# Kernel optimization log

Measured on AMD Instinct MI355X. Metric: run time of the kernel, lower is better.

The kernel has to match this reference:

```python
import jax, jax.numpy as jnp
import numpy as np

D, HEADS, HD, L, P, DFF = 256, 8, 32, 4, 4, 2048
B, NQ = 4, 900
SHAPES = [(128, 128), (64, 64), (32, 32), (16, 16)]
S = sum(h * w for h, w in SHAPES)


def setup_inputs():
    ks = iter(jax.random.split(jax.random.key(0), 20))
    rn = lambda *s: jax.random.normal(next(ks), s, jnp.float32) * 0.02
    cxcy = jax.random.uniform(next(ks), (B, NQ, 1, 2), minval=0.1, maxval=0.9)
    wh = jax.random.uniform(next(ks), (B, NQ, 1, 2), minval=0.05, maxval=0.3)
    ref = jnp.broadcast_to(jnp.concatenate([cxcy, wh], -1), (B, NQ, L, 4))
    starts = np.cumsum([0] + [h * w for h, w in SHAPES[:-1]])
    return dict(
        query=jax.random.normal(next(ks), (B, NQ, D), jnp.float32),
        query_pos=jax.random.normal(next(ks), (B, NQ, D), jnp.float32),
        reference_points=ref,
        input_flatten=jax.random.normal(next(ks), (B, S, D), jnp.float32),
        input_spatial_shapes=jnp.array(SHAPES, jnp.int32),
        input_level_start_index=jnp.array(starts, jnp.int32),
        sa_in_w=rn(3, D, D), sa_in_b=jnp.zeros((3, D)),
        sa_out_w=rn(D, D), sa_out_b=jnp.zeros((D,)),
        norm1_g=jnp.ones((D,)), norm1_b=jnp.zeros((D,)),
        value_w=rn(D, D), value_b=jnp.zeros((D,)),
        off_w=rn(D, HEADS * L * P * 2),
        off_b=jax.random.uniform(next(ks), (HEADS * L * P * 2,), minval=-1.0, maxval=1.0),
        aw_w=rn(D, HEADS * L * P), aw_b=jnp.zeros((HEADS * L * P,)),
        ca_out_w=rn(D, D), ca_out_b=jnp.zeros((D,)),
        norm2_g=jnp.ones((D,)), norm2_b=jnp.zeros((D,)),
        lin1_w=rn(D, DFF), lin1_b=jnp.zeros((DFF,)),
        lin2_w=rn(DFF, D), lin2_b=jnp.zeros((D,)),
        norm3_g=jnp.ones((D,)), norm3_b=jnp.zeros((D,)),
    )


def _ln(x, g, b, eps=1e-5):
    m = x.mean(-1, keepdims=True)
    v = ((x - m) ** 2).mean(-1, keepdims=True)
    return (x - m) * jax.lax.rsqrt(v + eps) * g + b


def _msdeform(q, input_flatten, ref, shapes, starts, value_w, value_b,
              off_w, off_b, aw_w, aw_b, out_w, out_b):
    Bq, Nq, _ = q.shape
    # value: (B, heads, S, head_dim)
    v = (input_flatten @ value_w + value_b).reshape(Bq, -1, HEADS, HD).transpose(0, 2, 1, 3)
    off = (q @ off_w + off_b).reshape(Bq, Nq, HEADS, L, P, 2).transpose(0, 2, 1, 3, 4, 5)
    aw = jax.nn.softmax((q @ aw_w + aw_b).reshape(Bq, Nq, HEADS, L * P), axis=-1)
    aw = aw.reshape(Bq, Nq, HEADS, L, P).transpose(0, 2, 1, 3, 4)  # (B,H,Nq,L,P)
    refc = ref[:, None, :, :, None, :]  # (B,1,Nq,L,1,4)
    # box refs: center + offset/P * wh * 0.5  (Deformable-DETR convention)
    loc = refc[..., :2] + off / P * refc[..., 2:] * 0.5  # (B,H,Nq,L,P,2)
    out = jnp.zeros((Bq, HEADS, Nq, HD), q.dtype)
    for l, (H, W) in enumerate(shapes):
        vl = jax.lax.dynamic_slice_in_dim(v, starts[l], H * W, axis=2)  # (B,H,HW,hd)
        x = loc[:, :, :, l, :, 0] * W - 0.5  # align_corners=False pixel coords
        y = loc[:, :, :, l, :, 1] * H - 0.5
        x0, y0 = jnp.floor(x), jnp.floor(y)
        dx, dy = x - x0, y - y0

        def g(xi, yi):
            valid = (xi >= 0) & (xi < W) & (yi >= 0) & (yi < H)  # zero padding
            idx = (jnp.clip(yi, 0, H - 1) * W + jnp.clip(xi, 0, W - 1)).astype(jnp.int32)
            gat = jnp.take_along_axis(vl, idx.reshape(Bq, HEADS, Nq * P, 1), axis=2)
            return gat.reshape(Bq, HEADS, Nq, P, HD) * valid[..., None]

        samp = (((1 - dx) * (1 - dy))[..., None] * g(x0, y0)
                + (dx * (1 - dy))[..., None] * g(x0 + 1, y0)
                + ((1 - dx) * dy)[..., None] * g(x0, y0 + 1)
                + (dx * dy)[..., None] * g(x0 + 1, y0 + 1))
        out = out + jnp.sum(aw[:, :, :, l, :, None] * samp, axis=3)
    return out.transpose(0, 2, 1, 3).reshape(Bq, Nq, D) @ out_w + out_b


def _layer(query, query_pos, reference_points, input_flatten, shapes, starts, p):
    Bq, Nq, _ = query.shape
    qk = query + query_pos
    heads = lambda x: x.reshape(Bq, Nq, HEADS, HD).transpose(0, 2, 1, 3)
    qh = heads(qk @ p['sa_in_w'][0] + p['sa_in_b'][0])
    kh = heads(qk @ p['sa_in_w'][1] + p['sa_in_b'][1])
    vh = heads(query @ p['sa_in_w'][2] + p['sa_in_b'][2])
    attn = jax.nn.softmax(jnp.einsum('bhqd,bhkd->bhqk', qh, kh) * (HD ** -0.5), axis=-1)
    sa = jnp.einsum('bhqk,bhkd->bhqd', attn, vh).transpose(0, 2, 1, 3).reshape(Bq, Nq, D)
    sa = sa @ p['sa_out_w'] + p['sa_out_b']
    x = _ln(query + sa, p['norm1_g'], p['norm1_b'])
    ca = _msdeform(x + query_pos, input_flatten, reference_points, shapes, starts,
                   p['value_w'], p['value_b'], p['off_w'], p['off_b'],
                   p['aw_w'], p['aw_b'], p['ca_out_w'], p['ca_out_b'])
    x = _ln(x + ca, p['norm2_g'], p['norm2_b'])
    ffn = jax.nn.relu(x @ p['lin1_w'] + p['lin1_b']) @ p['lin2_w'] + p['lin2_b']
    return _ln(x + ffn, p['norm3_g'], p['norm3_b'])


PNAMES = ['sa_in_w', 'sa_in_b', 'sa_out_w', 'sa_out_b', 'norm1_g', 'norm1_b',
          'value_w', 'value_b', 'off_w', 'off_b', 'aw_w', 'aw_b',
          'ca_out_w', 'ca_out_b', 'norm2_g', 'norm2_b',
          'lin1_w', 'lin1_b', 'lin2_w', 'lin2_b', 'norm3_g', 'norm3_b']


def reference(query, query_pos, reference_points, input_flatten,
              input_spatial_shapes, input_level_start_index,
              sa_in_w, sa_in_b, sa_out_w, sa_out_b, norm1_g, norm1_b,
              value_w, value_b, off_w, off_b, aw_w, aw_b,
              ca_out_w, ca_out_b, norm2_g, norm2_b,
              lin1_w, lin1_b, lin2_w, lin2_b, norm3_g, norm3_b):
    # spatial shapes / start indices are static structural metadata
    shapes = [(int(h), int(w)) for h, w in np.asarray(input_spatial_shapes)]
    starts = [int(s) for s in np.asarray(input_level_start_index)]
    p = dict(zip(PNAMES, (sa_in_w, sa_in_b, sa_out_w, sa_out_b, norm1_g, norm1_b,
                          value_w, value_b, off_w, off_b, aw_w, aw_b,
                          ca_out_w, ca_out_b, norm2_g, norm2_b,
                          lin1_w, lin1_b, lin2_w, lin2_b, norm3_g, norm3_b)))
    return _layer(query, query_pos, reference_points, input_flatten, shapes, starts, p)
```

## Files before the change

kernel.cpp:

```cpp
#include <hip/hip_runtime.h>
#include <hip/hip_bf16.h>

#define DD   256
#define NH   8
#define HDIM 32
#define LV   4
#define NP   4
#define DFF  2048
#define BB   4
#define NQQ  900
#define SS   21760

typedef __bf16 bf16x8 __attribute__((ext_vector_type(8)));
typedef __bf16 bf16x2 __attribute__((ext_vector_type(2)));
typedef float  f32x4  __attribute__((ext_vector_type(4)));

__device__ inline void stval(float* p, float v) { *p = v; }
__device__ inline void stval(__bf16* p, float v) { *p = (__bf16)v; }

struct TPtrs {
    const float* s[10];
    __bf16* d[10];
};

__global__ void transp_all(TPtrs P) {
    const int Ks[10] = {256, 256, 256, 256, 256, 256, 256, 256, 256, 2048};
    const int Ns[10] = {256, 256, 256, 256, 256, 256, 128, 256, 2048, 256};
    const int tiles[10] = {64, 64, 64, 64, 64, 64, 32, 64, 512, 512};
    int t = blockIdx.x;
    int j = 0, base = 0;
    while (t >= base + tiles[j]) { base += tiles[j]; j++; }
    int lt = t - base;
    int K = Ks[j], N = Ns[j];
    int tn = N >> 5;
    int nb = (lt % tn) * 32, kb = (lt / tn) * 32;
    const float* W = P.s[j];
    __bf16* Wt = P.d[j];
    __shared__ float tbuf[32][33];
    for (int i = threadIdx.y; i < 32; i += 8)
        tbuf[i][threadIdx.x] = W[(size_t)(kb + i) * N + nb + threadIdx.x];
    __syncthreads();
    for (int i = threadIdx.y; i < 32; i += 8)
        Wt[(size_t)(nb + i) * K + kb + threadIdx.x] = (__bf16)tbuf[threadIdx.x][i];
}

#define BM 64
#define BN 64
#define BKK 64

template <typename AT, typename OT, int RELU, int NSUB>
__global__ __launch_bounds__(256) void mfma_gemm(
    const AT* __restrict__ A, const float* __restrict__ A2,
    const __bf16* __restrict__ Wt,
    const float* __restrict__ bias, const float* __restrict__ bias2, int nsplit,
    OT* __restrict__ C, int M, int N, int K) {
    int tid = threadIdx.x;
    int lane = tid & 63;
    int wave = tid >> 6;
    int wr = wave >> 1, wc = wave & 1;
    int m0 = blockIdx.y * BM;
    int n0 = blockIdx.x * (BN * NSUB);

    __shared__ __attribute__((aligned(16))) __bf16 As[BM * BKK];
    __shared__ __attribute__((aligned(16))) __bf16 Bs[NSUB][BN * BKK];

    f32x4 acc[NSUB][2][2] = {};

    int srow = tid >> 2;
    int sq = tid & 3;
    int u0 = sq << 1;
    int p0 = (u0 ^ (srow & 7)) * 8;
    int p1 = ((u0 + 1) ^ (srow & 7)) * 8;
    int fr = lane & 15, gq = lane >> 4;

    for (int k0 = 0; k0 < K; k0 += BKK) {
        {
            int gm = m0 + srow;
            bf16x8 v0 = {}, v1 = {};
            if (gm < M) {
                if constexpr (sizeof(AT) == 4) {
                    const float* ap = (const float*)A + (size_t)gm * K + k0 + sq * 16;
                    f32x4 f0 = *(const f32x4*)(ap + 0);
                    f32x4 f1 = *(const f32x4*)(ap + 4);
                    f32x4 f2 = *(const f32x4*)(ap + 8);
                    f32x4 f3 = *(const f32x4*)(ap + 12);
                    if (A2) {
                        const float* ap2 = A2 + (size_t)gm * K + k0 + sq * 16;
                        f0 += *(const f32x4*)(ap2 + 0);
                        f1 += *(const f32x4*)(ap2 + 4);
                        f2 += *(const f32x4*)(ap2 + 8);
                        f3 += *(const f32x4*)(ap2 + 12);
                    }
#pragma unroll
                    for (int e = 0; e < 4; e++) {
                        v0[e] = (__bf16)f0[e]; v0[e + 4] = (__bf16)f1[e];
                        v1[e] = (__bf16)f2[e]; v1[e + 4] = (__bf16)f3[e];
                    }
                } else {
                    const __bf16* ap = (const __bf16*)A + (size_t)gm * K + k0 + sq * 16;
                    v0 = *(const bf16x8*)(ap);
                    v1 = *(const bf16x8*)(ap + 8);
                }
            }
            *(bf16x8*)(&As[srow * 64 + p0]) = v0;
            *(bf16x8*)(&As[srow * 64 + p1]) = v1;
        }
#pragma unroll
        for (int ns = 0; ns < NSUB; ns++) {
            int gn = n0 + ns * BN + srow;
            const __bf16* bp = Wt + (size_t)gn * K + k0 + sq * 16;
            bf16x8 w0 = *(const bf16x8*)(bp);
            bf16x8 w1 = *(const bf16x8*)(bp + 8);
            *(bf16x8*)(&Bs[ns][srow * 64 + p0]) = w0;
            *(bf16x8*)(&Bs[ns][srow * 64 + p1]) = w1;
        }
        __syncthreads();
#pragma unroll
        for (int ks = 0; ks < 2; ks++) {
            bf16x8 a[2];
#pragma unroll
            for (int i = 0; i < 2; i++) {
                int ma = wr * 32 + i * 16 + fr;
                a[i] = *(const bf16x8*)(&As[ma * 64 + ((ks * 4 + gq) ^ (ma & 7)) * 8]);
            }
#pragma unroll
            for (int ns = 0; ns < NSUB; ns++) {
                bf16x8 b[2];
#pragma unroll
                for (int j = 0; j < 2; j++) {
                    int nb = wc * 32 + j * 16 + fr;
                    b[j] = *(const bf16x8*)(&Bs[ns][nb * 64 + ((ks * 4 + gq) ^ (nb & 7)) * 8]);
                }
#pragma unroll
                for (int i = 0; i < 2; i++)
#pragma unroll
                    for (int j = 0; j < 2; j++)
                        acc[ns][i][j] = __builtin_amdgcn_mfma_f32_16x16x32_bf16(a[i], b[j], acc[ns][i][j], 0, 0, 0);
            }
        }
        __syncthreads();
    }
    int orow = gq * 4;
#pragma unroll
    for (int ns = 0; ns < NSUB; ns++)
#pragma unroll
        for (int i = 0; i < 2; i++)
#pragma unroll
            for (int j = 0; j < 2; j++) {
                int gn = n0 + ns * BN + wc * 32 + j * 16 + fr;
                float bv = (gn < nsplit) ? bias[gn] : bias2[gn - nsplit];
#pragma unroll
                for (int r = 0; r < 4; r++) {
                    int gm = m0 + wr * 32 + i * 16 + orow + r;
                    if (gm < M) {
                        float v = acc[ns][i][j][r] + bv;
                        if (RELU) v = fmaxf(v, 0.f);
                        stval(C + (size_t)gm * N + gn, v);
                    }
                }
            }
}

__global__ void fillmark(float* o, int n, float v) {
    int i = blockIdx.x * blockDim.x + threadIdx.x;
    if (i < n) o[i] = v;
}

__global__ void ln_res(const float* a, const float* b,
                       const float* g, const float* be, float* o) {
    int row = blockIdx.x;
    int t = threadIdx.x;
    float x = a[(size_t)row * DD + t] + b[(size_t)row * DD + t];
    __shared__ float red[DD];
    red[t] = x;
    __syncthreads();
    for (int s = 128; s > 0; s >>= 1) {
        if (t < s) red[t] += red[t + s];
        __syncthreads();
    }
    float m = red[0] * (1.f / DD);
    __syncthreads();
    float d0 = x - m;
    red[t] = d0 * d0;
    __syncthreads();
    for (int s = 128; s > 0; s >>= 1) {
        if (t < s) red[t] += red[t + s];
        __syncthreads();
    }
    float v = red[0] * (1.f / DD);
    o[(size_t)row * DD + t] = d0 * rsqrtf(v + 1e-5f) * g[t] + be[t];
}

#define QT 64
#define KT 64
#define NT ((NQQ + KT - 1) / KT)
#define QKLD 512

__global__ __launch_bounds__(256) void sa_attn_mfma(
    const __bf16* __restrict__ QK, const __bf16* __restrict__ V,
    float* __restrict__ O) {
    int blk = blockIdx.x;
    int tq = blk % NT;
    int bh = blk / NT;
    int h = bh % NH;
    int b = bh / NH;
    int tid = threadIdx.x;
    int lane = tid & 63;
    int wave = tid >> 6;
    int fr = lane & 15, gq = lane >> 4;
    int q0 = tq * QT;

    __shared__ __attribute__((aligned(16))) __bf16 Ks[KT][56];
    __shared__ __attribute__((aligned(16))) __bf16 Vt[HDIM][72];
    __shared__ __attribute__((aligned(16))) __bf16 Ps[4][16][72];

    int qrow = q0 + wave * 16 + fr;
    bf16x8 aq = {};
    if (qrow < NQQ)
        aq = *(const bf16x8*)(QK + ((size_t)(b * NQQ + qrow)) * QKLD + h * HDIM + gq * 8);

    f32x4 o0 = {}, o1 = {};
    float m_r[4] = {-1e30f, -1e30f, -1e30f, -1e30f};
    float l_r[4] = {0.f, 0.f, 0.f, 0.f};
    const float scale = 0.17677669529663687f;

    for (int kt = 0; kt < NT; kt++) {
        int kv0 = kt * KT;
        {
            int r = tid >> 2;
            int c8 = (tid & 3) * 8;
            int kvr = kv0 + r;
            bf16x8 kv_ = {}, vv_ = {};
            if (kvr < NQQ) {
                kv_ = *(const bf16x8*)(QK + ((size_t)(b * NQQ + kvr)) * QKLD + 256 + h * HDIM + c8);
                vv_ = *(const bf16x8*)(V + ((size_t)(b * NQQ + kvr)) * DD + h * HDIM + c8);
            }
            *(bf16x8*)(&Ks[r][c8]) = kv_;
#pragma unroll
            for (int j = 0; j < 8; j++) Vt[c8 + j][r] = vv_[j];
        }
        __syncthreads();

        f32x4 s[4];
#pragma unroll
        for (int f = 0; f < 4; f++) {
            bf16x8 bk = *(const bf16x8*)(&Ks[f * 16 + fr][gq * 8]);
            f32x4 z = {};
            s[f] = __builtin_amdgcn_mfma_f32_16x16x32_bf16(aq, bk, z, 0, 0, 0);
        }
#pragma unroll
        for (int f = 0; f < 4; f++) {
            bool valid = (kv0 + f * 16 + fr) < NQQ;
#pragma unroll
            for (int r = 0; r < 4; r++)
                s[f][r] = valid ? s[f][r] * scale : -1e30f;
        }
        float sc_[4];
#pragma unroll
        for (int r = 0; r < 4; r++) {
            float v = fmaxf(fmaxf(s[0][r], s[1][r]), fmaxf(s[2][r], s[3][r]));
            v = fmaxf(v, __shfl_xor(v, 1));
            v = fmaxf(v, __shfl_xor(v, 2));
            v = fmaxf(v, __shfl_xor(v, 4));
            v = fmaxf(v, __shfl_xor(v, 8));
            float mn = fmaxf(m_r[r], v);
            sc_[r] = expf(m_r[r] - mn);
            m_r[r] = mn;
        }
        float rs[4] = {0.f, 0.f, 0.f, 0.f};
#pragma unroll
        for (int f = 0; f < 4; f++)
#pragma unroll
            for (int r = 0; r < 4; r++) {
                float e = expf(s[f][r] - m_r[r]);
                s[f][r] = e;
                rs[r] += e;
            }
#pragma unroll
        for (int r = 0; r < 4; r++) {
            float v = rs[r];
            v += __shfl_xor(v, 1);
            v += __shfl_xor(v, 2);
            v += __shfl_xor(v, 4);
            v += __shfl_xor(v, 8);
            l_r[r] = l_r[r] * sc_[r] + v;
            o0[r] *= sc_[r];
            o1[r] *= sc_[r];
        }
#pragma unroll
        for (int f = 0; f < 4; f++)
#pragma unroll
            for (int r = 0; r < 4; r++)
                Ps[wave][gq * 4 + r][f * 16 + fr] = (__bf16)s[f][r];
#pragma unroll
        for (int c = 0; c < 2; c++) {
            bf16x8 ap = *(const bf16x8*)(&Ps[wave][fr][c * 32 + gq * 8]);
            bf16x8 bv0 = *(const bf16x8*)(&Vt[fr][c * 32 + gq * 8]);
            bf16x8 bv1 = *(const bf16x8*)(&Vt[16 + fr][c * 32 + gq * 8]);
            o0 = __builtin_amdgcn_mfma_f32_16x16x32_bf16(ap, bv0, o0, 0, 0, 0);
            o1 = __builtin_amdgcn_mfma_f32_16x16x32_bf16(ap, bv1, o1, 0, 0, 0);
        }
        __syncthreads();
    }
#pragma unroll
    for (int r = 0; r < 4; r++) {
        int qr = q0 + wave * 16 + gq * 4 + r;
        if (qr < NQQ) {
            float inv = 1.f / l_r[r];
            O[((size_t)(b * NQQ + qr)) * DD + h * HDIM + fr] = o0[r] * inv;
            O[((size_t)(b * NQQ + qr)) * DD + h * HDIM + 16 + fr] = o1[r] * inv;
        }
    }
}

#define OAW 384

__global__ __launch_bounds__(256) void msdeform3(
    const __bf16* __restrict__ val, const __bf16* __restrict__ oa,
    const float* __restrict__ ref, float* __restrict__ out) {
    int tid = threadIdx.x;
    int row = blockIdx.x;
    int b_ = row / NQQ;

    __shared__ float sx[128], sy[128], sw[128];

    if (tid < 128) {
        int h = tid >> 4;
        int lp = tid & 15;
        int l = lp >> 2;
        float logit = (float)oa[(size_t)row * OAW + 256 + h * 16 + lp];
        float ox = (float)oa[(size_t)row * OAW + h * 32 + lp * 2];
        float oy = (float)oa[(size_t)row * OAW + h * 32 + lp * 2 + 1];
        const float* rp = ref + ((size_t)row * LV + l) * 4;
        float cx = rp[0], cy = rp[1], rw = rp[2], rh = rp[3];
        float mv = logit;
        mv = fmaxf(mv, __shfl_xor(mv, 1));
        mv = fmaxf(mv, __shfl_xor(mv, 2));
        mv = fmaxf(mv, __shfl_xor(mv, 4));
        mv = fmaxf(mv, __shfl_xor(mv, 8));
        float e = expf(logit - mv);
        float sum = e;
        sum += __shfl_xor(sum, 1);
        sum += __shfl_xor(sum, 2);
        sum += __shfl_xor(sum, 4);
        sum += __shfl_xor(sum, 8);
        int Wl = 128 >> l;
        float lx = cx + ox * (1.0f / NP) * rw * 0.5f;
        float ly = cy + oy * (1.0f / NP) * rh * 0.5f;
        sx[tid] = lx * Wl - 0.5f;
        sy[tid] = ly * Wl - 0.5f;
        sw[tid] = e / sum;
    }
    __syncthreads();

    int cpar = tid & 7;
    int dgrp = (tid >> 3) & 3;
    int h = tid >> 5;
    const int stt[4] = {0, 16384, 20480, 21504};
    const __bf16* vb = val + (size_t)b_ * SS * DD + h * HDIM + dgrp * 8;
    float facc[8] = {};
#pragma unroll
    for (int k = 0; k < 8; k++) {
        int combo = cpar * 8 + k;
        int lp = combo >> 2;
        int tap = combo & 3;
        int l = lp >> 2;
        int Wl = 128 >> l;
        int cidx = h * 16 + lp;
        float x = sx[cidx], y = sy[cidx], w = sw[cidx];
        float x0f = floorf(x), y0f = floorf(y);
        float dx = x - x0f, dy = y - y0f;
        int xi = (int)x0f + (tap & 1);
        int yi = (int)y0f + (tap >> 1);
        float wt = ((tap & 1) ? dx : 1.f - dx) * ((tap >> 1) ? dy : 1.f - dy) * w;
        if ((xi >= 0) & (xi < Wl) & (yi >= 0) & (yi < Wl)) {
            bf16x8 t = *(const bf16x8*)(vb + (size_t)(stt[l] + yi * Wl + xi) * DD);
#pragma unroll
            for (int e = 0; e < 8; e++) facc[e] += wt * (float)t[e];
        }
    }
#pragma unroll
    for (int e = 0; e < 8; e++) {
        facc[e] += __shfl_xor(facc[e], 1);
        facc[e] += __shfl_xor(facc[e], 2);
        facc[e] += __shfl_xor(facc[e], 4);
    }
    float v = facc[0];
#pragma unroll
    for (int e = 1; e < 8; e++) if (cpar == e) v = facc[e];
    out[(size_t)row * DD + tid] = v;
}

extern "C" void kernel_launch(void* const* d_in, const int* in_sizes, int n_in,
                              void* d_out, int out_size, void* d_ws, size_t ws_size,
                              hipStream_t stream) {
    const float* query      = (const float*)d_in[0];
    const float* query_pos  = (const float*)d_in[1];
    const float* refpts     = (const float*)d_in[2];
    const float* input_flat = (const float*)d_in[3];
    const float* sa_in_w    = (const float*)d_in[6];
    const float* sa_in_b    = (const float*)d_in[7];
    const float* sa_out_w   = (const float*)d_in[8];
    const float* sa_out_b   = (const float*)d_in[9];
    const float* norm1_g    = (const float*)d_in[10];
    const float* norm1_b    = (const float*)d_in[11];
    const float* value_w    = (const float*)d_in[12];
    const float* value_b    = (const float*)d_in[13];
    const float* off_w      = (const float*)d_in[14];
    const float* off_b      = (const float*)d_in[15];
    const float* aw_w       = (const float*)d_in[16];
    const float* aw_b       = (const float*)d_in[17];
    const float* ca_out_w   = (const float*)d_in[18];
    const float* ca_out_b   = (const float*)d_in[19];
    const float* norm2_g    = (const float*)d_in[20];
    const float* norm2_b    = (const float*)d_in[21];
    const float* lin1_w     = (const float*)d_in[22];
    const float* lin1_b     = (const float*)d_in[23];
    const float* lin2_w     = (const float*)d_in[24];
    const float* lin2_b     = (const float*)d_in[25];
    const float* norm3_g    = (const float*)d_in[26];
    const float* norm3_b    = (const float*)d_in[27];
    float* out = (float*)d_out;

    const int M = BB * NQQ;
    const int NE = M * DD;
    const size_t slotBytes = (size_t)NE * 4;
    const size_t wElems = 6 * 65536 + 32768 + 65536 + 2 * 524288;
    const size_t wBytes = wElems * 2;
    const size_t bigBytes = (size_t)BB * SS * DD * 2;
    const size_t needBytes = 3 * slotBytes + wBytes + bigBytes;
    if (ws_size < needBytes) {
        float mark = 1000.0f + (float)(ws_size >> 20);
        fillmark<<<(out_size + 255) / 256, 256, 0, stream>>>(out, out_size, mark);
        return;
    }

    char* wsb = (char*)d_ws;
    float* s0 = (float*)(wsb);
    float* s1 = (float*)(wsb + slotBytes);
    float* s2 = (float*)(wsb + 2 * slotBytes);
    __bf16* wb = (__bf16*)(wsb + 3 * slotBytes);
    __bf16* vbig = (__bf16*)(wsb + 3 * slotBytes + wBytes);

    __bf16* wt_q   = wb;
    __bf16* wt_k   = wb + 65536;
    __bf16* wt_v   = wb + 131072;
    __bf16* wt_sa  = wb + 196608;
    __bf16* wt_val = wb + 262144;
    __bf16* wt_off = wb + 327680;
    __bf16* wt_aw  = wb + 393216;
    __bf16* wt_ca  = wb + 425984;
    __bf16* wt_l1  = wb + 491520;
    __bf16* wt_l2  = wb + 1015808;

    TPtrs tp;
    tp.s[0] = sa_in_w;          tp.d[0] = wt_q;
    tp.s[1] = sa_in_w + 65536;  tp.d[1] = wt_k;
    tp.s[2] = sa_in_w + 131072; tp.d[2] = wt_v;
    tp.s[3] = sa_out_w;         tp.d[3] = wt_sa;
    tp.s[4] = value_w;          tp.d[4] = wt_val;
    tp.s[5] = off_w;            tp.d[5] = wt_off;
    tp.s[6] = aw_w;             tp.d[6] = wt_aw;
    tp.s[7] = ca_out_w;         tp.d[7] = wt_ca;
    tp.s[8] = lin1_w;           tp.d[8] = wt_l1;
    tp.s[9] = lin2_w;           tp.d[9] = wt_l2;
    transp_all<<<1504, dim3(32, 8), 0, stream>>>(tp);

    __bf16* qkbuf = (__bf16*)s1;
    __bf16* Vp = (__bf16*)s2;
    __bf16* oabuf = (__bf16*)s1;

    const int mt = (M + BM - 1) / BM;
    const int mtv = (BB * SS) / BM;
    const int BIG = 1 << 30;

    mfma_gemm<float, __bf16, 0, 1><<<dim3(8, mt), 256, 0, stream>>>(
        query, query_pos, wt_q, sa_in_b, sa_in_b, BIG, qkbuf, M, 512, DD);
    mfma_gemm<float, __bf16, 0, 1><<<dim3(4, mt), 256, 0, stream>>>(
        query, nullptr, wt_v, sa_in_b + 512, sa_in_b, BIG, Vp, M, DD, DD);
    sa_attn_mfma<<<BB * NH * NT, 256, 0, stream>>>(qkbuf, Vp, s0);
    mfma_gemm<float, float, 0, 1><<<dim3(4, mt), 256, 0, stream>>>(
        s0, nullptr, wt_sa, sa_out_b, sa_out_b, BIG, s1, M, DD, DD);
    ln_res<<<M, DD, 0, stream>>>(query, s1, norm1_g, norm1_b, s2);
    mfma_gemm<float, __bf16, 0, 4><<<dim3(1, mtv), 256, 0, stream>>>(
        input_flat, nullptr, wt_val, value_b, value_b, BIG, vbig, BB * SS, DD, DD);
    mfma_gemm<float, __bf16, 0, 1><<<dim3(6, mt), 256, 0, stream>>>(
        s2, query_pos, wt_off, off_b, aw_b, 256, oabuf, M, OAW, DD);
    msdeform3<<<M, 256, 0, stream>>>(vbig, oabuf, refpts, s0);
    mfma_gemm<float, float, 0, 1><<<dim3(4, mt), 256, 0, stream>>>(
        s0, nullptr, wt_ca, ca_out_b, ca_out_b, BIG, s1, M, DD, DD);
    ln_res<<<M, DD, 0, stream>>>(s2, s1, norm2_g, norm2_b, s1);
    mfma_gemm<float, __bf16, 1, 1><<<dim3(32, mt), 256, 0, stream>>>(
        s1, nullptr, wt_l1, lin1_b, lin1_b, BIG, vbig, M, DFF, DD);
    mfma_gemm<__bf16, float, 0, 1><<<dim3(4, mt), 256, 0, stream>>>(
        vbig, nullptr, wt_l2, lin2_b, lin2_b, BIG, s0, M, DD, DFF);
    ln_res<<<M, DD, 0, stream>>>(s1, s0, norm3_g, norm3_b, out);
}
```

Before: 220.2 us.

## Add specialized double-buffered value projection GEMM with direct global-to-LDS weight loads

Replaces the generic templated GEMM for the large value projection (B*S x 256 x 256) with a dedicated kernel. It double-buffers the A and B tiles in shared memory, loads the bf16 weights straight into LDS with global_load_lds, and prefetches the next fp32 A chunk into registers while the MFMAs of the current chunk run, using XOR swizzling to avoid bank conflicts. The aim is to hide global memory latency on the largest GEMM in the layer. The cost is heavier LDS use (about 80KB per block), which may reduce occupancy, and the kernel assumes M is a multiple of 64 with no bounds checks.

```diff
diff --git a/kernel.cpp b/kernel.cpp
--- a/kernel.cpp
+++ b/kernel.cpp
@@ -17,6 +17,12 @@
 
 __device__ inline void stval(float* p, float v) { *p = v; }
 __device__ inline void stval(__bf16* p, float v) { *p = (__bf16)v; }
+
+__device__ __forceinline__ void gload16(const void* g, void* l) {
+    __builtin_amdgcn_global_load_lds(
+        (const __attribute__((address_space(1))) void*)g,
+        (__attribute__((address_space(3))) void*)l, 16, 0, 0);
+}
 
 struct TPtrs {
     const float* s[10];
@@ -157,6 +163,119 @@
                         if (RELU) v = fmaxf(v, 0.f);
                         stval(C + (size_t)gm * N + gn, v);
                     }
+                }
+            }
+}
+
+__global__ __launch_bounds__(256) void value_gemm(
+    const float* __restrict__ A, const __bf16* __restrict__ Wt,
+    const float* __restrict__ bias, __bf16* __restrict__ C) {
+    int tid = threadIdx.x;
+    int lane = tid & 63;
+    int wave = tid >> 6;
+    int wr = wave >> 1, wc = wave & 1;
+    int m0 = blockIdx.x * 64;
+
+    __shared__ __attribute__((aligned(16))) __bf16 As[2][64 * 64];
+    __shared__ __attribute__((aligned(16))) __bf16 Bs[2][4][64 * 64];
+
+    f32x4 acc[4][2][2] = {};
+
+    int srow = tid >> 2;
+    int sq = tid & 3;
+    int u0 = sq << 1;
+    int p0 = (u0 ^ (srow & 7)) * 8;
+    int p1 = ((u0 + 1) ^ (srow & 7)) * 8;
+    int fr = lane & 15, gq = lane >> 4;
+
+    int c_row = lane >> 3;
+    int c_u = lane & 7;
+    int gu = c_u ^ c_row;
+    const __bf16* bsrc0 = Wt + (size_t)(wave * 64 + c_row) * 256 + gu * 8;
+
+    const float* aptr = A + (size_t)(m0 + srow) * 256 + sq * 16;
+
+    f32x4 fa0 = *(const f32x4*)(aptr + 0);
+    f32x4 fa1 = *(const f32x4*)(aptr + 4);
+    f32x4 fa2 = *(const f32x4*)(aptr + 8);
+    f32x4 fa3 = *(const f32x4*)(aptr + 12);
+#pragma unroll
+    for (int c = 0; c < 8; c++)
+        gload16(bsrc0 + (size_t)c * 8 * 256, &Bs[0][wave][c * 512]);
+    {
+        bf16x8 v0, v1;
+#pragma unroll
+        for (int e = 0; e < 4; e++) {
+            v0[e] = (__bf16)fa0[e]; v0[e + 4] = (__bf16)fa1[e];
+            v1[e] = (__bf16)fa2[e]; v1[e + 4] = (__bf16)fa3[e];
+        }
+        *(bf16x8*)(&As[0][srow * 64 + p0]) = v0;
+        *(bf16x8*)(&As[0][srow * 64 + p1]) = v1;
+    }
+    __syncthreads();
+
+    for (int step = 0; step < 4; step++) {
+        int p = step & 1;
+        if (step < 3) {
+            const float* ap2 = aptr + (step + 1) * 64;
+            fa0 = *(const f32x4*)(ap2 + 0);
+            fa1 = *(const f32x4*)(ap2 + 4);
+            fa2 = *(const f32x4*)(ap2 + 8);
+            fa3 = *(const f32x4*)(ap2 + 12);
+            const __bf16* bsrc = bsrc0 + (step + 1) * 64;
+#pragma unroll
+            for (int c = 0; c < 8; c++)
+                gload16(bsrc + (size_t)c * 8 * 256, &Bs[p ^ 1][wave][c * 512]);
+        }
+#pragma unroll
+        for (int ks = 0; ks < 2; ks++) {
+            bf16x8 a[2];
+#pragma unroll
+            for (int i = 0; i < 2; i++) {
+                int ma = wr * 32 + i * 16 + fr;
+                a[i] = *(const bf16x8*)(&As[p][ma * 64 + ((ks * 4 + gq) ^ (ma & 7)) * 8]);
+            }
+#pragma unroll
+            for (int ns = 0; ns < 4; ns++) {
+                bf16x8 b[2];
+#pragma unroll
+                for (int j = 0; j < 2; j++) {
+                    int nb = wc * 32 + j * 16 + fr;
+                    b[j] = *(const bf16x8*)(&Bs[p][ns][nb * 64 + ((ks * 4 + gq) ^ (nb & 7)) * 8]);
+                }
+#pragma unroll
+                for (int i = 0; i < 2; i++)
+#pragma unroll
+                    for (int j = 0; j < 2; j++)
+                        acc[ns][i][j] = __builtin_amdgcn_mfma_f32_16x16x32_bf16(a[i], b[j], acc[ns][i][j], 0, 0, 0);
+            }
+        }
+        if (step < 3) {
+            bf16x8 v0, v1;
+#pragma unroll
+            for (int e = 0; e < 4; e++) {
+                v0[e] = (__bf16)fa0[e]; v0[e + 4] = (__bf16)fa1[e];
+                v1[e] = (__bf16)fa2[e]; v1[e + 4] = (__bf16)fa3[e];
+            }
+            *(bf16x8*)(&As[p ^ 1][srow * 64 + p0]) = v0;
+            *(bf16x8*)(&As[p ^ 1][srow * 64 + p1]) = v1;
+        }
+        __syncthreads();
+    }
+
+    int orow = gq * 4;
+#pragma unroll
+    for (int ns = 0; ns < 4; ns++)
+#pragma unroll
+        for (int i = 0; i < 2; i++)
+#pragma unroll
+            for (int j = 0; j < 2; j++) {
+                int gn = ns * 64 + wc * 32 + j * 16 + fr;
+                float bv = bias[gn];
+#pragma unroll
+                for (int r = 0; r < 4; r++) {
+                    int gm = m0 + wr * 32 + i * 16 + orow + r;
+                    C[(size_t)gm * 256 + gn] = (__bf16)(acc[ns][i][j][r] + bv);
                 }
             }
 }
@@ -482,8 +601,7 @@
     mfma_gemm<float, float, 0, 1><<<dim3(4, mt), 256, 0, stream>>>(
         s0, nullptr, wt_sa, sa_out_b, sa_out_b, BIG, s1, M, DD, DD);
     ln_res<<<M, DD, 0, stream>>>(query, s1, norm1_g, norm1_b, s2);
-    mfma_gemm<float, __bf16, 0, 4><<<dim3(1, mtv), 256, 0, stream>>>(
-        input_flat, nullptr, wt_val, value_b, value_b, BIG, vbig, BB * SS, DD, DD);
+    value_gemm<<<mtv, 256, 0, stream>>>(input_flat, wt_val, value_b, vbig);
     mfma_gemm<float, __bf16, 0, 1><<<dim3(6, mt), 256, 0, stream>>>(
         s2, query_pos, wt_off, off_b, aw_b, 256, oabuf, M, OAW, DD);
     msdeform3<<<M, 256, 0, stream>>>(vbig, oabuf, refpts, s0);
```

Result: no change. 217.0 us (-1.4%).
